# Kernel optimization log

Hardware: AMD Instinct MI355X
Metric: run time of the kernel (lower is better)

The kernel has to match this reference:

```python
import jax, jax.numpy as jnp
import numpy as np

RATE = 0.1
INPUT_SHAPE = [8192]
BATCH_DIMS = 1
K = max(1, round(RATE * int(np.prod(INPUT_SHAPE))))  # 819


def setup_inputs() -> dict:
    key = jax.random.key(0)
    x = jax.random.normal(key, (4096, 8192), dtype=jnp.float32)
    return {"x": x}


def reference(x) -> jnp.ndarray:
    batch_flat = int(np.prod(x.shape[:BATCH_DIMS]))
    x_flat = x.reshape(batch_flat, -1)            # [B, D]
    ax = jnp.abs(x_flat)
    topk_vals, _ = jax.lax.top_k(ax, K)           # [B, K] sorted descending
    thr = topk_vals[:, -1:]                        # kth largest |x| per row
    mask = (ax >= thr).reshape(x.shape)
    return jnp.where(mask, x, jnp.zeros_like(x))
```

## Files before the change

### kernel.cpp

```cpp
#include <hip/hip_runtime.h>
#include <stdint.h>


constexpr int NCOLS = 8192;
constexpr int TPB   = 256;
constexpr int V4    = NCOLS / 4;
constexpr int VPT   = V4 / TPB;

constexpr int PAD = 8;
constexpr int W1  = 1024;
constexpr int S1  = W1 + PAD;
constexpr int C1  = 2;
constexpr int B2  = 1024;
constexpr int S2  = B2 + PAD;
constexpr int HW  = (C1 * S1 > S2) ? C1 * S1 : S2;

constexpr int CAND_MAX = 2048;

struct Shared {
  uint32_t hist[HW];
  uint32_t cand[CAND_MAX];
  uint32_t wavesum[4];
  uint32_t digit;
  uint32_t rem;
  uint32_t cnt;
};

template <int BPT>
__device__ __forceinline__ uint32_t pick_winner(Shared& sh, const uint32_t (&hb)[BPT],
                                                uint32_t& rem, int tid, int lane, int wave) {
  uint32_t L = 0;
#pragma unroll
  for (int j = 0; j < BPT; ++j) L += hb[j];

  uint32_t suf = L;
#pragma unroll
  for (int off = 1; off < 64; off <<= 1) {
    uint32_t o = __shfl_down(suf, off, 64);
    suf += (lane + off < 64) ? o : 0u;
  }
  if (lane == 0) sh.wavesum[wave] = suf;
  __syncthreads();
  uint32_t addw = 0;
#pragma unroll
  for (int w = 0; w < 4; ++w) addw += (w > wave) ? sh.wavesum[w] : 0u;
  suf += addw;

  uint32_t s = suf - L;
#pragma unroll
  for (int j = BPT - 1; j >= 0; --j) {
    uint32_t snext = s;
    s += hb[j];
    if (s >= rem && snext < rem) {
      sh.digit = (uint32_t)(tid * BPT + j);
      sh.rem = rem - snext;
    }
  }
  __syncthreads();
  uint32_t d = sh.digit;
  rem = sh.rem;
  return d;
}

__device__ __forceinline__ uint32_t phase1(Shared& sh, const uint4 (&v)[VPT],
                                           uint32_t& rem, int tid, int lane, int wave) {
  uint4* hz = (uint4*)sh.hist;
  constexpr int ZW4 = (C1 * S1) / 4;
  for (int i = tid; i < ZW4; i += TPB) hz[i] = make_uint4(0u, 0u, 0u, 0u);
  if (tid == 0) sh.cnt = 0;
  __syncthreads();

  uint32_t* h = &sh.hist[(wave >> 1) * S1];
#pragma unroll
  for (int i = 0; i < VPT; ++i) {
    uint32_t a[4] = {v[i].x, v[i].y, v[i].z, v[i].w};
#pragma unroll
    for (int j = 0; j < 4; ++j) {
      uint32_t d = (a[j] & 0x7fffffffu) >> 20;
      atomicAdd(&h[d & (W1 - 1)], 1u << ((d >> 10) << 4));
    }
  }
  __syncthreads();

  constexpr int BPT = 2048 / TPB;
  uint32_t hb[BPT];
#pragma unroll
  for (int j = 0; j < BPT; ++j) hb[j] = 0;
  const int wbase = (tid & 127) * BPT;
  const int shift = (tid >> 7) << 4;
#pragma unroll
  for (int c = 0; c < C1; ++c) {
    const uint4* hp = (const uint4*)&sh.hist[c * S1 + wbase];
#pragma unroll
    for (int q = 0; q < BPT / 4; ++q) {
      uint4 t = hp[q];
      hb[4 * q + 0] += (t.x >> shift) & 0xffffu;
      hb[4 * q + 1] += (t.y >> shift) & 0xffffu;
      hb[4 * q + 2] += (t.z >> shift) & 0xffffu;
      hb[4 * q + 3] += (t.w >> shift) & 0xffffu;
    }
  }
  return pick_winner<BPT>(sh, hb, rem, tid, lane, wave);
}

template <bool FILTER>
__device__ __forceinline__ uint32_t phase_list(Shared& sh, int dshift,
                                               uint32_t d2match, uint32_t total,
                                               uint32_t& rem, int tid, int lane, int wave) {
  uint4* hz = (uint4*)sh.hist;
  constexpr int ZW4 = S2 / 4;
  for (int i = tid; i < ZW4; i += TPB) hz[i] = make_uint4(0u, 0u, 0u, 0u);
  __syncthreads();

  for (uint32_t p = tid; p < total; p += TPB) {
    uint32_t key = sh.cand[p];
    if (!FILTER || (((key >> 10) & 1023u) == d2match))
      atomicAdd(&sh.hist[(key >> dshift) & (B2 - 1)], 1u);
  }
  __syncthreads();

  constexpr int BPT = B2 / TPB;
  uint32_t hb[BPT];
  const uint4 t = *(const uint4*)&sh.hist[tid * BPT];
  hb[0] = t.x; hb[1] = t.y; hb[2] = t.z; hb[3] = t.w;
  return pick_winner<BPT>(sh, hb, rem, tid, lane, wave);
}

__device__ __forceinline__ uint32_t phase23_full(Shared& sh, const uint4 (&v)[VPT],
                                                 int dshift, int cshift, uint32_t cprefix,
                                                 uint32_t& rem, int tid, int lane, int wave) {
  uint4* hz = (uint4*)sh.hist;
  constexpr int ZW4 = S2 / 4;
  for (int i = tid; i < ZW4; i += TPB) hz[i] = make_uint4(0u, 0u, 0u, 0u);
  __syncthreads();

#pragma unroll
  for (int i = 0; i < VPT; ++i) {
    uint32_t a[4] = {v[i].x, v[i].y, v[i].z, v[i].w};
#pragma unroll
    for (int j = 0; j < 4; ++j) {
      uint32_t key = a[j] & 0x7fffffffu;
      if ((key >> cshift) == cprefix)
        atomicAdd(&sh.hist[(key >> dshift) & (B2 - 1)], 1u);
    }
  }
  __syncthreads();

  constexpr int BPT = B2 / TPB;
  uint32_t hb[BPT];
  const uint4 t = *(const uint4*)&sh.hist[tid * BPT];
  hb[0] = t.x; hb[1] = t.y; hb[2] = t.z; hb[3] = t.w;
  return pick_winner<BPT>(sh, hb, rem, tid, lane, wave);
}

__global__ __launch_bounds__(TPB, 4) void topk_row_kernel(const float* __restrict__ x,
                                                          float* __restrict__ out,
                                                          int K) {
  __shared__ Shared sh;
  const int row  = blockIdx.x;
  const int tid  = threadIdx.x;
  const int lane = tid & 63;
  const int wave = tid >> 6;

  const uint4* xr = (const uint4*)(x) + (size_t)row * V4;
  uint4 v[VPT];
#pragma unroll
  for (int i = 0; i < VPT; ++i) v[i] = xr[tid + i * TPB];

#pragma unroll
  for (int i = 0; i < VPT; ++i)
    asm volatile("" : "+v"(v[i].x), "+v"(v[i].y), "+v"(v[i].z), "+v"(v[i].w));

  uint32_t rem = (uint32_t)K;
  uint32_t d1 = phase1(sh, v, rem, tid, lane, wave);

#pragma unroll
  for (int i = 0; i < VPT; ++i) {
    uint32_t a[4] = {v[i].x, v[i].y, v[i].z, v[i].w};
#pragma unroll
    for (int j = 0; j < 4; ++j) {
      uint32_t key = a[j] & 0x7fffffffu;
      if ((key >> 20) == d1) {
        uint32_t p = atomicAdd(&sh.cnt, 1u);
        if (p < (uint32_t)CAND_MAX) sh.cand[p] = key;
      }
    }
  }
  __syncthreads();
  const uint32_t total = sh.cnt;

  uint32_t d2, d3;
  if (total <= (uint32_t)CAND_MAX) {
    d2 = phase_list<false>(sh, 10, 0, total, rem, tid, lane, wave);
    d3 = phase_list<true>(sh, 0, d2, total, rem, tid, lane, wave);
  } else {
    d2 = phase23_full(sh, v, 10, 20, d1, rem, tid, lane, wave);
    d3 = phase23_full(sh, v, 0, 10, (d1 << 10) | d2, rem, tid, lane, wave);
  }

  const uint32_t thr = (d1 << 20) | (d2 << 10) | d3;

  uint4* outr = (uint4*)(out) + (size_t)row * V4;
#pragma unroll
  for (int i = 0; i < VPT; ++i) {
    uint4 o = v[i];
    o.x = ((o.x & 0x7fffffffu) >= thr) ? o.x : 0u;
    o.y = ((o.y & 0x7fffffffu) >= thr) ? o.y : 0u;
    o.z = ((o.z & 0x7fffffffu) >= thr) ? o.z : 0u;
    o.w = ((o.w & 0x7fffffffu) >= thr) ? o.w : 0u;
    outr[tid + i * TPB] = o;
  }
}

extern "C" void kernel_launch(void* const* d_in, const int* in_sizes, int n_in,
                              void* d_out, int out_size, void* d_ws, size_t ws_size,
                              hipStream_t stream) {
  (void)n_in; (void)out_size; (void)d_ws; (void)ws_size;
  const float* x = (const float*)d_in[0];
  float* out = (float*)d_out;
  const int rows = in_sizes[0] / NCOLS;
  const int K = (int)(0.1 * NCOLS + 0.5);
  topk_row_kernel<<<rows, TPB, 0, stream>>>(x, out, K);
}
```

Measured before the change: 233.4 us.

## Use 8 phase-1 histogram copies and ballot-based per-wave candidate compaction

Phase 1 now spreads histogram atomics over 8 padded LDS copies selected by thread group instead of 2 per wave pair, and sums the packed 16-bit counters before unpacking. Candidate collection replaces a single shared atomic counter with wave-ballot prefix compaction into per-wave 256-entry segments. The aim is to cut LDS atomic contention. In exchange it uses more LDS for zeroing and reduction, which may lower occupancy, and it falls back to the full rescan more often because the per-wave segments are small.

```diff
diff --git a/kernel.cpp b/kernel.cpp
--- a/kernel.cpp
+++ b/kernel.cpp
@@ -7,23 +7,22 @@
 constexpr int V4    = NCOLS / 4;
 constexpr int VPT   = V4 / TPB;
 
-constexpr int PAD = 8;
 constexpr int W1  = 1024;
-constexpr int S1  = W1 + PAD;
-constexpr int C1  = 2;
+constexpr int S1  = 1036;
+constexpr int C1  = 8;
 constexpr int B2  = 1024;
-constexpr int S2  = B2 + PAD;
-constexpr int HW  = (C1 * S1 > S2) ? C1 * S1 : S2;
-
-constexpr int CAND_MAX = 2048;
+constexpr int S2  = B2 + 8;
+constexpr int HW  = C1 * S1;
+
+constexpr int CSEG = 256;
 
 struct Shared {
   uint32_t hist[HW];
-  uint32_t cand[CAND_MAX];
+  uint32_t cand[4 * CSEG];
+  uint32_t segcnt[4];
   uint32_t wavesum[4];
   uint32_t digit;
   uint32_t rem;
-  uint32_t cnt;
 };
 
 template <int BPT>
@@ -67,10 +66,9 @@
   uint4* hz = (uint4*)sh.hist;
   constexpr int ZW4 = (C1 * S1) / 4;
   for (int i = tid; i < ZW4; i += TPB) hz[i] = make_uint4(0u, 0u, 0u, 0u);
-  if (tid == 0) sh.cnt = 0;
-  __syncthreads();
-
-  uint32_t* h = &sh.hist[(wave >> 1) * S1];
+  __syncthreads();
+
+  uint32_t* h = &sh.hist[((tid >> 3) & 7) * S1];
 #pragma unroll
   for (int i = 0; i < VPT; ++i) {
     uint32_t a[4] = {v[i].x, v[i].y, v[i].z, v[i].w};
@@ -83,39 +81,41 @@
   __syncthreads();
 
   constexpr int BPT = 2048 / TPB;
-  uint32_t hb[BPT];
-#pragma unroll
-  for (int j = 0; j < BPT; ++j) hb[j] = 0;
   const int wbase = (tid & 127) * BPT;
   const int shift = (tid >> 7) << 4;
+  uint32_t ws[BPT];
+#pragma unroll
+  for (int j = 0; j < BPT; ++j) ws[j] = 0;
 #pragma unroll
   for (int c = 0; c < C1; ++c) {
     const uint4* hp = (const uint4*)&sh.hist[c * S1 + wbase];
-#pragma unroll
-    for (int q = 0; q < BPT / 4; ++q) {
-      uint4 t = hp[q];
-      hb[4 * q + 0] += (t.x >> shift) & 0xffffu;
-      hb[4 * q + 1] += (t.y >> shift) & 0xffffu;
-      hb[4 * q + 2] += (t.z >> shift) & 0xffffu;
-      hb[4 * q + 3] += (t.w >> shift) & 0xffffu;
-    }
-  }
+    uint4 t0 = hp[0], t1 = hp[1];
+    ws[0] += t0.x; ws[1] += t0.y; ws[2] += t0.z; ws[3] += t0.w;
+    ws[4] += t1.x; ws[5] += t1.y; ws[6] += t1.z; ws[7] += t1.w;
+  }
+  uint32_t hb[BPT];
+#pragma unroll
+  for (int j = 0; j < BPT; ++j) hb[j] = (ws[j] >> shift) & 0xffffu;
   return pick_winner<BPT>(sh, hb, rem, tid, lane, wave);
 }
 
 template <bool FILTER>
 __device__ __forceinline__ uint32_t phase_list(Shared& sh, int dshift,
-                                               uint32_t d2match, uint32_t total,
+                                               uint32_t d2match,
                                                uint32_t& rem, int tid, int lane, int wave) {
   uint4* hz = (uint4*)sh.hist;
   constexpr int ZW4 = S2 / 4;
   for (int i = tid; i < ZW4; i += TPB) hz[i] = make_uint4(0u, 0u, 0u, 0u);
   __syncthreads();
 
-  for (uint32_t p = tid; p < total; p += TPB) {
-    uint32_t key = sh.cand[p];
-    if (!FILTER || (((key >> 10) & 1023u) == d2match))
-      atomicAdd(&sh.hist[(key >> dshift) & (B2 - 1)], 1u);
+#pragma unroll
+  for (int s = 0; s < 4; ++s) {
+    const uint32_t n = sh.segcnt[s];
+    for (uint32_t p = tid; p < n; p += TPB) {
+      uint32_t key = sh.cand[s * CSEG + p];
+      if (!FILTER || (((key >> 10) & 1023u) == d2match))
+        atomicAdd(&sh.hist[(key >> dshift) & (B2 - 1)], 1u);
+    }
   }
   __syncthreads();
 
@@ -174,25 +174,32 @@
   uint32_t rem = (uint32_t)K;
   uint32_t d1 = phase1(sh, v, rem, tid, lane, wave);
 
+  uint32_t wcnt = 0;
+  const uint32_t segbase = (uint32_t)wave * CSEG;
 #pragma unroll
   for (int i = 0; i < VPT; ++i) {
     uint32_t a[4] = {v[i].x, v[i].y, v[i].z, v[i].w};
 #pragma unroll
     for (int j = 0; j < 4; ++j) {
       uint32_t key = a[j] & 0x7fffffffu;
-      if ((key >> 20) == d1) {
-        uint32_t p = atomicAdd(&sh.cnt, 1u);
-        if (p < (uint32_t)CAND_MAX) sh.cand[p] = key;
-      }
-    }
-  }
-  __syncthreads();
-  const uint32_t total = sh.cnt;
+      bool m = ((key >> 20) == d1);
+      uint64_t mk = __ballot(m);
+      uint32_t pos = wcnt + (uint32_t)__popcll(mk & ((1ull << lane) - 1ull));
+      if (m && pos < (uint32_t)CSEG) sh.cand[segbase + pos] = key;
+      wcnt += (uint32_t)__popcll(mk);
+    }
+  }
+  if (lane == 0) sh.segcnt[wave] = wcnt;
+  __syncthreads();
+
+  bool ovf = false;
+#pragma unroll
+  for (int w = 0; w < 4; ++w) ovf |= (sh.segcnt[w] > (uint32_t)CSEG);
 
   uint32_t d2, d3;
-  if (total <= (uint32_t)CAND_MAX) {
-    d2 = phase_list<false>(sh, 10, 0, total, rem, tid, lane, wave);
-    d3 = phase_list<true>(sh, 0, d2, total, rem, tid, lane, wave);
+  if (!ovf) {
+    d2 = phase_list<false>(sh, 10, 0, rem, tid, lane, wave);
+    d3 = phase_list<true>(sh, 0, d2, rem, tid, lane, wave);
   } else {
     d2 = phase23_full(sh, v, 10, 20, d1, rem, tid, lane, wave);
     d3 = phase23_full(sh, v, 0, 10, (d1 << 10) | d2, rem, tid, lane, wave);
```

After: 232.6 us. No clear change (-0.3%).
